# Performance work log

Measured on AMD Instinct MI355X. Metric: run time of the kernel, lower is better.

The kernel has to match this reference:

```python
import jax, jax.numpy as jnp
import numpy as np

H = 100  # hidden_size
D = 300  # input/output feature dim (hardcoded in module)
T = 32768  # number of timesteps


def _lstm_layer(x_seq, W_ih, W_hh, b_ih, b_hh):
    """Single LSTM layer over time. x_seq: [T, H_in]. PyTorch gate order i,f,g,o."""
    Hh = W_hh.shape[1]
    b = b_ih + b_hh
    # precompute input projection for all timesteps (removes per-step GEMM)
    x_proj = x_seq @ W_ih.T + b  # [T, 4H]

    def step(carry, xp_t):
        h, c = carry
        gates = xp_t + h @ W_hh.T  # [4H]
        i, f, g, o = jnp.split(gates, 4, axis=-1)
        c = jax.nn.sigmoid(f) * c + jax.nn.sigmoid(i) * jnp.tanh(g)
        h = jax.nn.sigmoid(o) * jnp.tanh(c)
        return (h, c), h

    h0 = jnp.zeros((Hh,), x_seq.dtype)
    c0 = jnp.zeros((Hh,), x_seq.dtype)
    (h_T, c_T), hs = jax.lax.scan(step, (h0, c0), x_proj)
    return hs, h_T, c_T


def setup_inputs() -> dict:
    key = jax.random.key(0)
    ks = jax.random.split(key, 14)
    s = 0.08
    return {
        "inputs": jax.random.normal(ks[0], (T, D), jnp.float32),
        "W_inp": jax.random.normal(ks[1], (H, D), jnp.float32) * s,
        "b_inp": jax.random.normal(ks[2], (H,), jnp.float32) * s,
        "W_ih_l0": jax.random.normal(ks[3], (4 * H, H), jnp.float32) * s,
        "W_hh_l0": jax.random.normal(ks[4], (4 * H, H), jnp.float32) * s,
        "b_ih_l0": jax.random.normal(ks[5], (4 * H,), jnp.float32) * s,
        "b_hh_l0": jax.random.normal(ks[6], (4 * H,), jnp.float32) * s,
        "W_ih_l1": jax.random.normal(ks[7], (4 * H, H), jnp.float32) * s,
        "W_hh_l1": jax.random.normal(ks[8], (4 * H, H), jnp.float32) * s,
        "b_ih_l1": jax.random.normal(ks[9], (4 * H,), jnp.float32) * s,
        "b_hh_l1": jax.random.normal(ks[10], (4 * H,), jnp.float32) * s,
        "W_out": jax.random.normal(ks[11], (D, H), jnp.float32) * s,
        "b_out": jax.random.normal(ks[12], (D,), jnp.float32) * s,
    }


def reference(inputs, W_inp, b_inp, W_ih_l0, W_hh_l0, b_ih_l0, b_hh_l0,
              W_ih_l1, W_hh_l1, b_ih_l1, b_hh_l1, W_out, b_out):
    # teacher-forced forward (force=True): input projection for all steps at once
    x = inputs @ W_inp.T + b_inp  # [T, H]
    h0_seq, h0_T, c0_T = _lstm_layer(x, W_ih_l0, W_hh_l0, b_ih_l0, b_hh_l0)
    h1_seq, h1_T, c1_T = _lstm_layer(h0_seq, W_ih_l1, W_hh_l1, b_ih_l1, b_hh_l1)
    outputs = h1_seq @ W_out.T + b_out  # [T, D]
    h_n = jnp.stack([h0_T, h1_T])  # [2, H] final hidden per layer
    c_n = jnp.stack([c0_T, c1_T])  # [2, H] final cell per layer
    return outputs, h_n, c_n
```

## Files before the change

### kernel.cpp

```cpp
#include <hip/hip_runtime.h>

#define T_STEPS 32768
#define OUT_BASE 9830400

typedef _Float16 h2 __attribute__((ext_vector_type(2)));
#define H2BC(f_) __builtin_bit_cast(h2, f_)

#define ALD(p)     __hip_atomic_load((p), __ATOMIC_RELAXED, __HIP_MEMORY_SCOPE_AGENT)
#define AST(p, v)  __hip_atomic_store((p), (v), __ATOMIC_RELAXED, __HIP_MEMORY_SCOPE_AGENT)
#define ASTR(p, v) __hip_atomic_store((p), (v), __ATOMIC_RELEASE, __HIP_MEMORY_SCOPE_AGENT)
#define CFENCE()   asm volatile("" ::: "memory")

__device__ __forceinline__ float fdot2(h2 a, h2 b, float c) {
#if __has_builtin(__builtin_amdgcn_fdot2)
    return __builtin_amdgcn_fdot2(a, b, c, false);
#else
    return c + (float)a.x * (float)b.x + (float)a.y * (float)b.y;
#endif
}

__device__ __forceinline__ float sigf(float x) { return 1.f / (1.f + __expf(-x)); }

__device__ __forceinline__ float tanh_f(float x) {
    float a = fabsf(x);
    float e = __expf(-2.f * a);
    float t = (1.f - e) / (1.f + e);
    return x < 0.f ? -t : t;
}

template <int CTRL>
__device__ __forceinline__ float qperm(float x) {
#if __has_builtin(__builtin_amdgcn_update_dpp)
    return __builtin_bit_cast(
        float, __builtin_amdgcn_update_dpp(0, __builtin_bit_cast(int, x), CTRL, 0xF, 0xF, true));
#else
    return __shfl_xor(x, CTRL == 0xB1 ? 1 : (CTRL == 0x4E ? 2 : 3));
#endif
}

__device__ __forceinline__ void bar_lds() {
    asm volatile("s_waitcnt lgkmcnt(0)\n\ts_barrier" ::: "memory");
}

__device__ __forceinline__ void ldw(h2* w, const float* p) {
#pragma unroll
    for (int k = 0; k < 25; k++) {
        float2 v = ((const float2*)p)[k];
        h2 t; t.x = (_Float16)v.x; t.y = (_Float16)v.y; w[k] = t;
    }
}

__device__ __forceinline__ float2 mv25(const h2* wA, const h2* wB, const char* rec) {
    const float4* hv = (const float4*)rec;
    float pA = 0.f, pB = 0.f;
#pragma unroll
    for (int c = 0; c < 6; c++) {
        float4 v = hv[c];
        pA = fdot2(wA[4 * c + 0], H2BC(v.x), pA); pB = fdot2(wB[4 * c + 0], H2BC(v.x), pB);
        pA = fdot2(wA[4 * c + 1], H2BC(v.y), pA); pB = fdot2(wB[4 * c + 1], H2BC(v.y), pB);
        pA = fdot2(wA[4 * c + 2], H2BC(v.z), pA); pB = fdot2(wB[4 * c + 2], H2BC(v.z), pB);
        pA = fdot2(wA[4 * c + 3], H2BC(v.w), pA); pB = fdot2(wB[4 * c + 3], H2BC(v.w), pB);
    }
    float vl = *(const float*)(rec + 96);
    pA = fdot2(wA[24], H2BC(vl), pA); pB = fdot2(wB[24], H2BC(vl), pB);
    return make_float2(pA, pB);
}

__global__ void k_precomp(const float* __restrict__ W_inp, const float* __restrict__ b_inp,
                          const float* __restrict__ W_ih0, const float* __restrict__ b_ih0,
                          const float* __restrict__ b_hh0,
                          float* __restrict__ Wc, float* __restrict__ bc) {
    int idx = blockIdx.x * 256 + threadIdx.x;
    if (idx < 120000) {
        int r = idx / 300, d = idx % 300;
        float acc = 0.f;
        for (int h = 0; h < 100; h++) acc += W_ih0[r * 100 + h] * W_inp[h * 300 + d];
        Wc[idx] = acc;
    } else if (idx < 120400) {
        int r = idx - 120000;
        float acc = b_ih0[r] + b_hh0[r];
        for (int h = 0; h < 100; h++) acc += W_ih0[r * 100 + h] * b_inp[h];
        bc[r] = acc;
    }
}

__global__ __launch_bounds__(512) void k_xproj(const float* __restrict__ inp,
                                               const float* __restrict__ Wc,
                                               const float* __restrict__ bc,
                                               _Float16* __restrict__ x0p) {
    __shared__ float xs[32 * 300];
    int t0 = blockIdx.x * 32;
    for (int idx = threadIdx.x; idx < 9600; idx += 512) xs[idx] = inp[(size_t)t0 * 300 + idx];
    __syncthreads();
    int j = threadIdx.x;
    if (j < 400) {
        float acc[32];
#pragma unroll
        for (int i = 0; i < 32; i++) acc[i] = 0.f;
        const float4* w4 = (const float4*)(Wc + j * 300);
        const float4* x4 = (const float4*)xs;
        for (int d4 = 0; d4 < 75; d4++) {
            float4 w = w4[d4];
#pragma unroll
            for (int ti = 0; ti < 32; ti++) {
                float4 x = x4[ti * 75 + d4];
                acc[ti] += w.x * x.x + w.y * x.y + w.z * x.z + w.w * x.w;
            }
        }
        float bb = bc[j];
        int dst = (j % 100) * 4 + j / 100;
#pragma unroll
        for (int ti = 0; ti < 32; ti++)
            x0p[(size_t)(t0 + ti) * 400 + dst] = (_Float16)(acc[ti] + bb);
    }
}


#define B0TICK(T_, XR_, P_) do {                                                             \
    if (j < 400) {                                                                           \
        float xc_ = XR_;                                                                     \
        int tn_ = (T_) + 2 < T_STEPS ? (T_) + 2 : T_STEPS - 1;                               \
        XR_ = (float)x0p[(size_t)tn_ * 400 + j];                                             \
        float2 p_ = mv25(wA, wB, (const char*)lds[P_] + hoff);                               \
        float pA_ = p_.x + qperm<0xB1>(p_.x);                                                \
        float pB_ = p_.y + qperm<0xB1>(p_.y);                                                \
        float sv_ = (H ? pB_ : pA_) + xc_;                                                   \
        float nl_ = __builtin_fmaf(sigf(sv_ * s_), s_, addc_);                               \
        float fg_ = qperm<0xB1>(nl_), gg_ = qperm<0x4E>(nl_), og_ = qperm<0x1B>(nl_);        \
        if (q == 0) {                                                                        \
            c0 = fg_ * c0 + nl_ * gg_;                                                       \
            float h0v_ = og_ * tanh_f(c0);                                                   \
            ((_Float16*)lds[1 - (P_)])[hidx] = (_Float16)h0v_;                               \
            if ((T_) == T_STEPS - 1) { outTail[u] = h0v_; outTail[200 + u] = c0; }           \
        }                                                                                    \
    } else if (j >= 448) {                                                                   \
        if (kk < 50 && (T_) >= 1)                                                            \
            AST(&h0seq[(size_t)((T_) - 1) * 50 + kk], lds[P_][pidx]);                        \
        if (kk == 0 && (((T_) & 7) == 7)) ASTR(&flags[0], (unsigned)(T_));                   \
    }                                                                                        \
    bar_lds();                                                                               \
} while (0)

#define B1TICK(T_, P_, WREG_, LREG_) do {                                                    \
    if (j < 400) {                                                                           \
        const char* hb_ = (const char*)lds[P_];                                              \
        float2 p0_ = mv25(wA0, wB0, hb_ + hoff);                          \
        float2 p1_ = mv25(wA1, wB1, hb_ + 224 + hoff);                  \
        float pA_ = p0_.x + p1_.x;  pA_ += qperm<0xB1>(pA_);                                 \
        float pB_ = p0_.y + p1_.y;  pB_ += qperm<0xB1>(pB_);                                 \
        float sv_ = (H ? pB_ : pA_) + bz;                                                    \
        float nl_ = __builtin_fmaf(sigf(sv_ * s_), s_, addc_);                               \
        float fg_ = qperm<0xB1>(nl_), gg_ = qperm<0x4E>(nl_), og_ = qperm<0x1B>(nl_);        \
        if (q == 0) {                                                                        \
            c1 = fg_ * c1 + nl_ * gg_;                                                       \
            float h1v_ = og_ * tanh_f(c1);                                                   \
            ((_Float16*)(lds[1 - (P_)] + 56))[hidx] = (_Float16)h1v_;                        \
            h1s[(size_t)(T_) * 100 + u] = h1v_;                                              \
            if ((T_) == T_STEPS - 1) { outTail[100 + u] = h1v_; outTail[300 + u] = c1; }     \
        }                                                                                    \
    } else if (j >= 448) {                                                                   \
        if (kk < 50) {                                                                       \
            if ((T_) + 1 < T_STEPS) lds[1 - (P_)][pidx] = WREG_;                             \
            if ((T_) + 2 < T_STEPS) {                                                        \
                unsigned need_ = (unsigned)(T_) + 3u;                                        \
                if (fcache < need_) {                                                        \
                    unsigned f_;                                                             \
                    while ((f_ = ALD(flags)) < need_) __builtin_amdgcn_s_sleep(2);           \
                    fcache = f_;                                                             \
                    CFENCE();                                                                \
                }                                                                            \
                LREG_ = ALD(&h0seq[(size_t)((T_) + 2) * 50 + kk]);                           \
            }                                                                                \
        }                                                                                    \
    }                                                                                        \
    bar_lds();                                                                               \
} while (0)

__global__ __launch_bounds__(512) __attribute__((amdgpu_waves_per_eu(2, 2)))
void k_scan2(const _Float16* __restrict__ x0p,
             const float* __restrict__ Whh0,
             const float* __restrict__ Wih1,
             const float* __restrict__ Whh1,
             const float* __restrict__ bih1,
             const float* __restrict__ bhh1,
             float* __restrict__ h1s,
             float* __restrict__ outTail,
             unsigned* __restrict__ h0seq,
             unsigned* __restrict__ flags) {
    __shared__ __align__(16) unsigned lds[2][112];
    const int j = threadIdx.x;
    const int q = j & 3, u = j >> 2, H = q & 1, gA = (q >> 1) * 2;
    const int hoff = H * 112;
    const int hidx = (u < 50) ? u : 56 + (u - 50);
    const int kk = j - 448;
    const int pidx = (kk < 25) ? kk : kk + 3;
    const float s_ = (q == 2) ? 2.f : 1.f;
    const float addc_ = (q == 2) ? -1.f : 0.f;

    if (blockIdx.x == 0) {
        h2 wA[25], wB[25];
        float xa = 0.f, xb = 0.f, c0 = 0.f;
        if (j < 400) {
            int r0 = gA * 100 + u;
            ldw(wA, Whh0 + r0 * 100 + 50 * H);
            ldw(wB, Whh0 + (r0 + 100) * 100 + 50 * H);
            xa = (float)x0p[j];
            xb = (float)x0p[400 + j];
        }
        if (j < 224) ((unsigned*)lds)[j] = 0u;
        __syncthreads();

        for (int t = 0; t < T_STEPS; t += 2) {
            B0TICK(t, xa, 0);
            B0TICK(t + 1, xb, 1);
        }
        if (j >= 448) {
            if (kk < 50) AST(&h0seq[(size_t)(T_STEPS - 1) * 50 + kk], lds[0][pidx]);
            if (kk == 0) ASTR(&flags[0], (unsigned)T_STEPS);
        }
    } else {
        h2 wA0[25], wB0[25], wA1[25], wB1[25];
        float bz = 0.f, c1 = 0.f;
        unsigned vA = 0, vB = 0, fcache = 0;
        if (j < 400) {
            int r0 = gA * 100 + u;
            ldw(wA0, Wih1 + r0 * 100 + 50 * H);
            ldw(wB0, Wih1 + (r0 + 100) * 100 + 50 * H);
            ldw(wA1, Whh1 + r0 * 100 + 50 * H);
            ldw(wB1, Whh1 + (r0 + 100) * 100 + 50 * H);
            int ro = q * 100 + u;
            bz = bih1[ro] + bhh1[ro];
        }
        if (j < 224) ((unsigned*)lds)[j] = 0u;
        __syncthreads();
        if (j >= 448) {
            unsigned f_;
            while ((f_ = ALD(flags)) < 2u) __builtin_amdgcn_s_sleep(8);
            fcache = f_;
            CFENCE();
            if (kk < 50) {
                vA = ALD(&h0seq[kk]);
                vB = ALD(&h0seq[50 + kk]);
                lds[0][pidx] = vA;
            }
        }
        __syncthreads();

        for (int t = 0; t < T_STEPS; t += 2) {
            B1TICK(t, 0, vB, vA);
            B1TICK(t + 1, 1, vA, vB);
        }
    }
}

__global__ __launch_bounds__(320) void k_out(const float* __restrict__ h1s,
                                             const float* __restrict__ Wout,
                                             const float* __restrict__ bout,
                                             float* __restrict__ out) {
    __shared__ float hs[32 * 100];
    int t0 = blockIdx.x * 32;
    for (int idx = threadIdx.x; idx < 3200; idx += 320) hs[idx] = h1s[(size_t)t0 * 100 + idx];
    __syncthreads();
    int d = threadIdx.x;
    if (d < 300) {
        float acc[32];
#pragma unroll
        for (int i = 0; i < 32; i++) acc[i] = 0.f;
        const float4* w4 = (const float4*)(Wout + d * 100);
        const float4* h4 = (const float4*)hs;
        for (int j4 = 0; j4 < 25; j4++) {
            float4 w = w4[j4];
#pragma unroll
            for (int ti = 0; ti < 32; ti++) {
                float4 h = h4[ti * 25 + j4];
                acc[ti] += w.x * h.x + w.y * h.y + w.z * h.z + w.w * h.w;
            }
        }
        float bb = bout[d];
#pragma unroll
        for (int ti = 0; ti < 32; ti++) out[(size_t)(t0 + ti) * 300 + d] = acc[ti] + bb;
    }
}

extern "C" void kernel_launch(void* const* d_in, const int* in_sizes, int n_in,
                              void* d_out, int out_size, void* d_ws, size_t ws_size,
                              hipStream_t stream) {
    const float* inputs = (const float*)d_in[0];
    const float* W_inp  = (const float*)d_in[1];
    const float* b_inp  = (const float*)d_in[2];
    const float* W_ih0  = (const float*)d_in[3];
    const float* W_hh0  = (const float*)d_in[4];
    const float* b_ih0  = (const float*)d_in[5];
    const float* b_hh0  = (const float*)d_in[6];
    const float* W_ih1  = (const float*)d_in[7];
    const float* W_hh1  = (const float*)d_in[8];
    const float* b_ih1  = (const float*)d_in[9];
    const float* b_hh1  = (const float*)d_in[10];
    const float* W_out  = (const float*)d_in[11];
    const float* b_out  = (const float*)d_in[12];
    float* out = (float*)d_out;

    char* ws = (char*)d_ws;
    _Float16* x0p = (_Float16*)ws;
    float* h1s = (float*)(ws + 26214400);
    float* Wc  = (float*)(ws + 26214400 + 13107200);
    float* bc  = Wc + 120000;

    unsigned* h0seq = (unsigned*)out;
    unsigned* flagp = (unsigned*)out + 1638400;
    float* outTail = out + OUT_BASE;

    hipMemsetAsync(flagp, 0, 4, stream);
    k_precomp<<<471, 256, 0, stream>>>(W_inp, b_inp, W_ih0, b_ih0, b_hh0, Wc, bc);
    k_xproj<<<1024, 512, 0, stream>>>(inputs, Wc, bc, x0p);

    void* args[] = {(void*)&x0p, (void*)&W_hh0, (void*)&W_ih1, (void*)&W_hh1,
                    (void*)&b_ih1, (void*)&b_hh1, (void*)&h1s, (void*)&outTail,
                    (void*)&h0seq, (void*)&flagp};
    hipLaunchCooperativeKernel((void*)k_scan2, dim3(2), dim3(512), args, 0, stream);

    k_out<<<1024, 320, 0, stream>>>(h1s, W_out, b_out, out);
}
```

Before: 23.91 ms.

## Split layer-1 input projection into a third pipelined block via ring buffer

Adds a third cooperative block that computes the layer-1 input projection (W_ih1·h0 + bias) in 16-step chunks into a global ring buffer. The layer-1 recurrent block then only does the W_hh1 matvec plus a prefetched ring load per step. This halves the serial per-step matvec work on the layer-1 critical path. In exchange it adds flag-based handshakes between three blocks and extra global ring traffic, and the layer-1 block now lags layer 0 by at least a chunk.

```diff
diff --git a/kernel.cpp b/kernel.cpp
--- a/kernel.cpp
+++ b/kernel.cpp
@@ -2,6 +2,7 @@
 
 #define T_STEPS 32768
 #define OUT_BASE 9830400
+#define RMASK 16383
 
 typedef _Float16 h2 __attribute__((ext_vector_type(2)));
 #define H2BC(f_) __builtin_bit_cast(h2, f_)
@@ -121,7 +122,7 @@
         float xc_ = XR_;                                                                     \
         int tn_ = (T_) + 2 < T_STEPS ? (T_) + 2 : T_STEPS - 1;                               \
         XR_ = (float)x0p[(size_t)tn_ * 400 + j];                                             \
-        float2 p_ = mv25(wA, wB, (const char*)lds[P_] + hoff);                               \
+        float2 p_ = mv25(wA, wB, (const char*)(lds + (P_) * 112) + hoff);                    \
         float pA_ = p_.x + qperm<0xB1>(p_.x);                                                \
         float pB_ = p_.y + qperm<0xB1>(p_.y);                                                \
         float sv_ = (H ? pB_ : pA_) + xc_;                                                   \
@@ -130,54 +131,49 @@
         if (q == 0) {                                                                        \
             c0 = fg_ * c0 + nl_ * gg_;                                                       \
             float h0v_ = og_ * tanh_f(c0);                                                   \
-            ((_Float16*)lds[1 - (P_)])[hidx] = (_Float16)h0v_;                               \
+            ((_Float16*)(lds + (1 - (P_)) * 112))[hidx] = (_Float16)h0v_;                    \
             if ((T_) == T_STEPS - 1) { outTail[u] = h0v_; outTail[200 + u] = c0; }           \
         }                                                                                    \
     } else if (j >= 448) {                                                                   \
         if (kk < 50 && (T_) >= 1)                                                            \
-            AST(&h0seq[(size_t)((T_) - 1) * 50 + kk], lds[P_][pidx]);                        \
+            AST(&h0seq[(size_t)((T_) - 1) * 50 + kk], (lds + (P_) * 112)[pidx]);             \
         if (kk == 0 && (((T_) & 7) == 7)) ASTR(&flags[0], (unsigned)(T_));                   \
     }                                                                                        \
     bar_lds();                                                                               \
 } while (0)
 
-#define B1TICK(T_, P_, WREG_, LREG_) do {                                                    \
+#define B2TICK(T_, ZR_, P_) do {                                                             \
     if (j < 400) {                                                                           \
-        const char* hb_ = (const char*)lds[P_];                                              \
-        float2 p0_ = mv25(wA0, wB0, hb_ + hoff);                          \
-        float2 p1_ = mv25(wA1, wB1, hb_ + 224 + hoff);                  \
-        float pA_ = p0_.x + p1_.x;  pA_ += qperm<0xB1>(pA_);                                 \
-        float pB_ = p0_.y + p1_.y;  pB_ += qperm<0xB1>(pB_);                                 \
-        float sv_ = (H ? pB_ : pA_) + bz;                                                    \
+        float zc_ = ZR_;                                                                     \
+        int tn_ = (T_) + 2 < T_STEPS ? (T_) + 2 : T_STEPS - 1;                               \
+        ZR_ = ALD(&z1ring[(size_t)(tn_ & RMASK) * 400 + j]);                                 \
+        float2 p_ = mv25(wA, wB, (const char*)(lds + (P_) * 112) + hoff);                    \
+        float pA_ = p_.x + qperm<0xB1>(p_.x);                                                \
+        float pB_ = p_.y + qperm<0xB1>(p_.y);                                                \
+        float sv_ = (H ? pB_ : pA_) + zc_;              \
         float nl_ = __builtin_fmaf(sigf(sv_ * s_), s_, addc_);                               \
         float fg_ = qperm<0xB1>(nl_), gg_ = qperm<0x4E>(nl_), og_ = qperm<0x1B>(nl_);        \
         if (q == 0) {                                                                        \
             c1 = fg_ * c1 + nl_ * gg_;                                                       \
             float h1v_ = og_ * tanh_f(c1);                                                   \
-            ((_Float16*)(lds[1 - (P_)] + 56))[hidx] = (_Float16)h1v_;                        \
+            ((_Float16*)(lds + (1 - (P_)) * 112))[hidx] = (_Float16)h1v_;                    \
             h1s[(size_t)(T_) * 100 + u] = h1v_;                                              \
             if ((T_) == T_STEPS - 1) { outTail[100 + u] = h1v_; outTail[300 + u] = c1; }     \
         }                                                                                    \
-    } else if (j >= 448) {                                                                   \
-        if (kk < 50) {                                                                       \
-            if ((T_) + 1 < T_STEPS) lds[1 - (P_)][pidx] = WREG_;                             \
-            if ((T_) + 2 < T_STEPS) {                                                        \
-                unsigned need_ = (unsigned)(T_) + 3u;                                        \
-                if (fcache < need_) {                                                        \
-                    unsigned f_;                                                             \
-                    while ((f_ = ALD(flags)) < need_) __builtin_amdgcn_s_sleep(2);           \
-                    fcache = f_;                                                             \
-                    CFENCE();                                                                \
-                }                                                                            \
-                LREG_ = ALD(&h0seq[(size_t)((T_) + 2) * 50 + kk]);                           \
-            }                                                                                \
+    } else if (j == 448) {                                                                   \
+        int tq_ = (T_) + 3 < T_STEPS ? (T_) + 3 : T_STEPS - 1;                               \
+        unsigned need_ = (unsigned)(tq_ >> 4) + 1u;                                          \
+        if (zdc < need_) {                                                                   \
+            while ((zdc = ALD(&flags[1])) < need_) __builtin_amdgcn_s_sleep(2);              \
+            CFENCE();                                                                        \
         }                                                                                    \
+        if (((T_) & 255) == 255) ASTR(&flags[2], (unsigned)(T_) + 1u);                       \
     }                                                                                        \
     bar_lds();                                                                               \
 } while (0)
 
 __global__ __launch_bounds__(512) __attribute__((amdgpu_waves_per_eu(2, 2)))
-void k_scan2(const _Float16* __restrict__ x0p,
+void k_scan3(const _Float16* __restrict__ x0p,
              const float* __restrict__ Whh0,
              const float* __restrict__ Wih1,
              const float* __restrict__ Whh1,
@@ -186,8 +182,9 @@
              float* __restrict__ h1s,
              float* __restrict__ outTail,
              unsigned* __restrict__ h0seq,
+             float* __restrict__ z1ring,
              unsigned* __restrict__ flags) {
-    __shared__ __align__(16) unsigned lds[2][112];
+    __shared__ __align__(16) unsigned lds[16 * 56];
     const int j = threadIdx.x;
     const int q = j & 3, u = j >> 2, H = q & 1, gA = (q >> 1) * 2;
     const int hoff = H * 112;
@@ -207,7 +204,7 @@
             xa = (float)x0p[j];
             xb = (float)x0p[400 + j];
         }
-        if (j < 224) ((unsigned*)lds)[j] = 0u;
+        if (j < 224) lds[j] = 0u;
         __syncthreads();
 
         for (int t = 0; t < T_STEPS; t += 2) {
@@ -215,40 +212,77 @@
             B0TICK(t + 1, xb, 1);
         }
         if (j >= 448) {
-            if (kk < 50) AST(&h0seq[(size_t)(T_STEPS - 1) * 50 + kk], lds[0][pidx]);
+            if (kk < 50) AST(&h0seq[(size_t)(T_STEPS - 1) * 50 + kk], lds[pidx]);
             if (kk == 0) ASTR(&flags[0], (unsigned)T_STEPS);
         }
-    } else {
-        h2 wA0[25], wB0[25], wA1[25], wB1[25];
-        float bz = 0.f, c1 = 0.f;
-        unsigned vA = 0, vB = 0, fcache = 0;
+    } else if (blockIdx.x == 1) {
+        h2 wA[25], wB[25];
+        float bz = 0.f;
         if (j < 400) {
             int r0 = gA * 100 + u;
-            ldw(wA0, Wih1 + r0 * 100 + 50 * H);
-            ldw(wB0, Wih1 + (r0 + 100) * 100 + 50 * H);
-            ldw(wA1, Whh1 + r0 * 100 + 50 * H);
-            ldw(wB1, Whh1 + (r0 + 100) * 100 + 50 * H);
+            ldw(wA, Wih1 + r0 * 100 + 50 * H);
+            ldw(wB, Wih1 + (r0 + 100) * 100 + 50 * H);
             int ro = q * 100 + u;
             bz = bih1[ro] + bhh1[ro];
         }
-        if (j < 224) ((unsigned*)lds)[j] = 0u;
+        for (int idx = j; idx < 16 * 56; idx += 512) lds[idx] = 0u;
         __syncthreads();
-        if (j >= 448) {
-            unsigned f_;
-            while ((f_ = ALD(flags)) < 2u) __builtin_amdgcn_s_sleep(8);
-            fcache = f_;
+
+        unsigned fcache = 0, bpc = 0;
+        for (int tau = 0; tau < 2048; ++tau) {
+            const int t0 = tau * 16;
+            while (fcache < (unsigned)(t0 + 16)) {
+                fcache = ALD(&flags[0]);
+                if (fcache < (unsigned)(t0 + 16)) __builtin_amdgcn_s_sleep(8);
+            }
+            int lim = t0 + 32 - (RMASK + 1);
+            if (lim > 0) {
+                while ((int)bpc < lim) {
+                    bpc = ALD(&flags[2]);
+                    if ((int)bpc < lim) __builtin_amdgcn_s_sleep(8);
+                }
+            }
             CFENCE();
-            if (kk < 50) {
-                vA = ALD(&h0seq[kk]);
-                vB = ALD(&h0seq[50 + kk]);
-                lds[0][pidx] = vA;
-            }
-        }
+            for (int g = j; g < 800; g += 512) {
+                int tt = g / 50, k = g % 50;
+                lds[tt * 56 + ((k < 25) ? k : k + 3)] = ALD(&h0seq[(size_t)t0 * 50 + g]);
+            }
+            __syncthreads();
+            if (j < 400) {
+                for (int tt = 0; tt < 16; ++tt) {
+                    float2 p = mv25(wA, wB, (const char*)(lds + tt * 56) + hoff);
+                    float pA = p.x + qperm<0xB1>(p.x);
+                    float pB = p.y + qperm<0xB1>(p.y);
+                    AST(&z1ring[(size_t)((t0 + tt) & RMASK) * 400 + j], (H ? pB : pA) + bz);
+                }
+            }
+            __syncthreads();
+            if (j == 0) ASTR(&flags[1], (unsigned)(tau + 1));
+        }
+    } else {
+        h2 wA[25], wB[25];
+        float za = 0.f, zb = 0.f, c1 = 0.f;
+        unsigned zdc = 0;
+        if (j < 400) {
+            int r0 = gA * 100 + u;
+            ldw(wA, Whh1 + r0 * 100 + 50 * H);
+            ldw(wB, Whh1 + (r0 + 100) * 100 + 50 * H);
+        }
+        if (j < 224) lds[j] = 0u;
         __syncthreads();
+        if (j == 448) {
+            while ((zdc = ALD(&flags[1])) < 1u) __builtin_amdgcn_s_sleep(8);
+            CFENCE();
+        }
+        __syncthreads();
+        if (j < 400) {
+            za = ALD(&z1ring[j]);
+            zb = ALD(&z1ring[400 + j]);
+        }
 
         for (int t = 0; t < T_STEPS; t += 2) {
-            B1TICK(t, 0, vB, vA);
-            B1TICK(t + 1, 1, vA, vB);
+            B2TICK(t, za, 0);
+            B2TICK(t + 1, zb, 1);
         }
     }
 }
@@ -306,18 +340,19 @@
     float* Wc  = (float*)(ws + 26214400 + 13107200);
     float* bc  = Wc + 120000;
 
-    unsigned* h0seq = (unsigned*)out;
-    unsigned* flagp = (unsigned*)out + 1638400;
-    float* outTail = out + OUT_BASE;
-
-    hipMemsetAsync(flagp, 0, 4, stream);
+    float*    z1ring = out;
+    unsigned* h0seq  = (unsigned*)((char*)out + 26214400);
+    unsigned* flagsp = (unsigned*)((char*)out + 32768000);
+    float*    outTail = out + OUT_BASE;
+
+    hipMemsetAsync(flagsp, 0, 16, stream);
     k_precomp<<<471, 256, 0, stream>>>(W_inp, b_inp, W_ih0, b_ih0, b_hh0, Wc, bc);
     k_xproj<<<1024, 512, 0, stream>>>(inputs, Wc, bc, x0p);
 
     void* args[] = {(void*)&x0p, (void*)&W_hh0, (void*)&W_ih1, (void*)&W_hh1,
                     (void*)&b_ih1, (void*)&b_hh1, (void*)&h1s, (void*)&outTail,
-                    (void*)&h0seq, (void*)&flagp};
-    hipLaunchCooperativeKernel((void*)k_scan2, dim3(2), dim3(512), args, 0, stream);
+                    (void*)&h0seq, (void*)&z1ring, (void*)&flagsp};
+    hipLaunchCooperativeKernel((void*)k_scan3, dim3(3), dim3(512), args, 0, stream);
 
     k_out<<<1024, 320, 0, stream>>>(h1s, W_out, b_out, out);
 }
```

New measurement: 20.73 ms. -13.3%, faster.
